# Kernel optimization log

Measured on AMD Instinct MI355X. Metric: run time of the kernel, lower is better.

The kernel has to match this reference:

```python
import jax, jax.numpy as jnp
import numpy as np

B, L, H_IN = 2, 512, 768
E = 256          # hidden_size
N = 12           # num_labels


def setup_inputs() -> dict:
    key = jax.random.key(0)
    ks = jax.random.split(key, 10)
    lim_in = 1.0 / np.sqrt(H_IN)
    lim_e = 1.0 / np.sqrt(E)
    lim_2e = 1.0 / np.sqrt(2 * E)
    return {
        "x":    jax.random.normal(ks[0], (B, L, H_IN), dtype=jnp.float32),
        "sW":   jax.random.uniform(ks[1], (E, H_IN), jnp.float32, -lim_in, lim_in),
        "sb":   jax.random.uniform(ks[2], (E,), jnp.float32, -lim_in, lim_in),
        "tW":   jax.random.uniform(ks[3], (E, H_IN), jnp.float32, -lim_in, lim_in),
        "tb":   jax.random.uniform(ks[4], (E,), jnp.float32, -lim_in, lim_in),
        "f2W":  jax.random.uniform(ks[5], (E, 2 * E), jnp.float32, -lim_2e, lim_2e),
        "f2b":  jax.random.uniform(ks[6], (E,), jnp.float32, -lim_2e, lim_2e),
        "f3W":  jax.random.normal(ks[7], (N, E), dtype=jnp.float32),  # init_weights: normal_
        "f3b":  jax.random.uniform(ks[8], (N,), jnp.float32, -lim_e, lim_e),
        "blW":  jax.random.normal(ks[9], (E * N, E), dtype=jnp.float32),  # bi_linear, no bias
    }


def reference(x, sW, sb, tW, tb, f2W, f2b, f3W, f3b, blW):
    b, l, _ = x.shape
    s = jax.nn.relu(x @ sW.T + sb)  # [B,L,E]
    t = jax.nn.relu(x @ tW.T + tb)  # [B,L,E]
    # biaffine term: key[b,s,e,n] = (s @ blW.T) reshaped, then key @ t^T
    key = (s @ blW.T).reshape(b, l, E, N)             # [B,L,E,N]
    out1 = jnp.einsum('bsen,ble->bsnl', key, t)       # [B,S,N,L]
    # pairwise concat-MLP, decomposed: cat(u,v) @ f2W.T == u@Wu.T + v@Wv.T
    Wu, Wv = f2W[:, :E], f2W[:, E:]
    su = s @ Wu.T                                     # [B,L,E]
    tv = t @ Wv.T                                     # [B,L,E]
    h = jax.nn.relu(su[:, :, None, :] + tv[:, None, :, :] + f2b)  # [B,L,L,E]
    out2 = h @ f3W.T + f3b                            # [B,L,L,N]
    out2 = jnp.transpose(out2, (0, 1, 3, 2))          # [B,L,N,L]
    return out1 + out2
```

## Files before the change

kernel.cpp:

```cpp
#include <hip/hip_runtime.h>
#include <hip/hip_bf16.h>


typedef unsigned short u16;
typedef __attribute__((ext_vector_type(8))) short    s16x8;
typedef __attribute__((ext_vector_type(8))) _Float16 f16x8;
typedef __attribute__((ext_vector_type(4))) float    f32x4;

__device__ inline u16 f2h(float f) { return __builtin_bit_cast(u16, (_Float16)f); }

__device__ inline s16x8 cvt2(float4 a, float4 b) {
    f16x8 h;
    h[0] = (_Float16)a.x; h[1] = (_Float16)a.y; h[2] = (_Float16)a.z; h[3] = (_Float16)a.w;
    h[4] = (_Float16)b.x; h[5] = (_Float16)b.y; h[6] = (_Float16)b.z; h[7] = (_Float16)b.w;
    return __builtin_bit_cast(s16x8, h);
}

__device__ inline f16x8 relu8(f16x8 v) {
#if __has_builtin(__builtin_elementwise_max)
    f16x8 z = {};
    return __builtin_elementwise_max(v, z);
#else
#pragma unroll
    for (int q = 0; q < 8; ++q) v[q] = v[q] > (_Float16)0.f ? v[q] : (_Float16)0.f;
    return v;
#endif
}

__device__ inline f32x4 mfma_f16(s16x8 a, s16x8 b, f32x4 c) {
    return __builtin_amdgcn_mfma_f32_16x16x32_f16(
        __builtin_bit_cast(f16x8, a), __builtin_bit_cast(f16x8, b), c, 0, 0, 0);
}
__device__ inline f32x4 mfma_f16v(f16x8 a, s16x8 b, f32x4 c) {
    return __builtin_amdgcn_mfma_f32_16x16x32_f16(a, __builtin_bit_cast(f16x8, b), c, 0, 0, 0);
}

__global__ __launch_bounds__(256, 3)
void prep_kernel(const float* __restrict__ x, const float* __restrict__ sW,
                 const float* __restrict__ tW, const float* __restrict__ sb,
                 const float* __restrict__ tb, const float* __restrict__ f2W,
                 const float* __restrict__ blW, const float* __restrict__ f3W,
                 u16* __restrict__ STb, u16* __restrict__ blkw, u16* __restrict__ f3wb)
{
    if (blockIdx.x >= 256) {
        int idx = (blockIdx.x - 256) * 256 + threadIdx.x;
        float4 v;
        u16* dst;
        if (idx < 229376) {
            int i4 = idx * 4;
            int r = i4 >> 8, k = i4 & 255;
            const float* src;
            if (r < 3072)      { int n = r >> 8, e = r & 255; src = &blW[(e * 12 + n) * 256 + k]; }
            else if (r < 3328) { src = &f2W[(r - 3072) * 512 + k]; }
            else               { src = &f2W[(r - 3328) * 512 + 256 + k]; }
            v = *(const float4*)src;
            dst = &blkw[i4];
        } else {
            int i4 = (idx - 229376) * 4;
            int row = i4 >> 8, e = i4 & 255;
            if (row < 12) v = *(const float4*)&f3W[row * 256 + e];
            else          v = make_float4(0.f, 0.f, 0.f, 0.f);
            dst = &f3wb[i4];
        }
        ushort4 o;
        o.x = f2h(v.x); o.y = f2h(v.y); o.z = f2h(v.z); o.w = f2h(v.w);
        *(ushort4*)dst = o;
        return;
    }
    __shared__ u16 As[64 * 72];
    __shared__ u16 Bs[32 * 72];
    const int tid = threadIdx.x;
    const int g = blockIdx.x;
    const int xcd = g & 7, slot = g >> 3;
    const int m0 = (((xcd << 1) | (slot >> 4))) * 64;
    const int n0 = (slot & 15) * 32;
    const int w = tid >> 6, l = tid & 63;
    const int wr = (w >> 1) * 32, wc = (w & 1) * 16;
    const int lr = l & 15, lg = l >> 4;
    const int srow = tid >> 2, kq = tid & 3;

    const float* ap = &x[(size_t)(m0 + srow) * 768 + kq * 16];
    const bool bstg = (tid < 128);
    const float* bp = nullptr;
    if (bstg) {
        int br = n0 + (tid >> 2);
        bp = (br < 256) ? &sW[(size_t)br * 768 + kq * 16]
                        : &tW[(size_t)(br - 256) * 768 + kq * 16];
    }
    float4 ra0 = *(const float4*)(ap + 0),  ra1 = *(const float4*)(ap + 4);
    float4 ra2 = *(const float4*)(ap + 8),  ra3 = *(const float4*)(ap + 12);
    float4 rb0, rb1, rb2, rb3;
    if (bstg) {
        rb0 = *(const float4*)(bp + 0);  rb1 = *(const float4*)(bp + 4);
        rb2 = *(const float4*)(bp + 8);  rb3 = *(const float4*)(bp + 12);
    }

    f32x4 acc[2] = {};
    for (int k0 = 0; k0 < 768; k0 += 64) {
        __syncthreads();
        *(s16x8*)&As[srow * 72 + kq * 16]     = cvt2(ra0, ra1);
        *(s16x8*)&As[srow * 72 + kq * 16 + 8] = cvt2(ra2, ra3);
        if (bstg) {
            *(s16x8*)&Bs[(tid >> 2) * 72 + kq * 16]     = cvt2(rb0, rb1);
            *(s16x8*)&Bs[(tid >> 2) * 72 + kq * 16 + 8] = cvt2(rb2, rb3);
        }
        __syncthreads();
        if (k0 + 64 < 768) {
            ra0 = *(const float4*)(ap + k0 + 64 + 0);  ra1 = *(const float4*)(ap + k0 + 64 + 4);
            ra2 = *(const float4*)(ap + k0 + 64 + 8);  ra3 = *(const float4*)(ap + k0 + 64 + 12);
            if (bstg) {
                rb0 = *(const float4*)(bp + k0 + 64 + 0);  rb1 = *(const float4*)(bp + k0 + 64 + 4);
                rb2 = *(const float4*)(bp + k0 + 64 + 8);  rb3 = *(const float4*)(bp + k0 + 64 + 12);
            }
        }
#pragma unroll
        for (int kk = 0; kk < 64; kk += 32) {
            s16x8 af[2], bf;
            af[0] = *(const s16x8*)&As[(wr      + lr) * 72 + kk + lg * 8];
            af[1] = *(const s16x8*)&As[(wr + 16 + lr) * 72 + kk + lg * 8];
            bf    = *(const s16x8*)&Bs[(wc      + lr) * 72 + kk + lg * 8];
            acc[0] = mfma_f16(af[0], bf, acc[0]);
            acc[1] = mfma_f16(af[1], bf, acc[1]);
        }
    }
#pragma unroll
    for (int fi = 0; fi < 2; ++fi) {
#pragma unroll
        for (int r = 0; r < 4; ++r) {
            int grow = m0 + wr + fi * 16 + lg * 4 + r;
            int gcol = n0 + wc + lr;
            float bias = (gcol < 256) ? sb[gcol] : tb[gcol - 256];
            float v = fmaxf(acc[fi][r] + bias, 0.f);
            STb[(size_t)grow * 512 + gcol] = f2h(v);
        }
    }
}

__global__ __launch_bounds__(256, 6)
void gemm_kst(const u16* __restrict__ STb, const u16* __restrict__ BLKW,
              const float* __restrict__ f2b,
              u16* __restrict__ KEYF, u16* __restrict__ SUp, u16* __restrict__ TVp)
{
    __shared__ u16 As[64 * 72];
    __shared__ u16 Bs[64 * 72];
    const int tid = threadIdx.x;
    const int lin = blockIdx.x + blockIdx.y * 56;
    const int xcd = lin & 7, slot = lin >> 3;
    const int n0 = (xcd * 7 + (slot >> 4)) * 64;
    const int m0 = (slot & 15) * 64;
    const int w = tid >> 6, l = tid & 63;
    const int wr = (w >> 1) * 32, wc = (w & 1) * 32;
    const int lr = l & 15, lg = l >> 4;
    const int srow = tid >> 2, kq = tid & 3;

    const u16* A = STb + (n0 >= 3328 ? 256 : 0);
    const u16* ap = &A[(size_t)(m0 + srow) * 512];
    const u16* bp = &BLKW[(size_t)(n0 + srow) * 256];
    s16x8 ra0 = *(const s16x8*)&ap[kq * 8];
    s16x8 ra1 = *(const s16x8*)&ap[(kq + 4) * 8];
    s16x8 rb0 = *(const s16x8*)&bp[kq * 8];
    s16x8 rb1 = *(const s16x8*)&bp[(kq + 4) * 8];

    f32x4 acc[2][2] = {};
    for (int k0 = 0; k0 < 256; k0 += 64) {
        __syncthreads();
        *(s16x8*)&As[srow * 72 + kq * 8]       = ra0;
        *(s16x8*)&As[srow * 72 + (kq + 4) * 8] = ra1;
        *(s16x8*)&Bs[srow * 72 + kq * 8]       = rb0;
        *(s16x8*)&Bs[srow * 72 + (kq + 4) * 8] = rb1;
        __syncthreads();
        if (k0 + 64 < 256) {
            ra0 = *(const s16x8*)&ap[k0 + 64 + kq * 8];
            ra1 = *(const s16x8*)&ap[k0 + 64 + (kq + 4) * 8];
            rb0 = *(const s16x8*)&bp[k0 + 64 + kq * 8];
            rb1 = *(const s16x8*)&bp[k0 + 64 + (kq + 4) * 8];
        }
#pragma unroll
        for (int kk = 0; kk < 64; kk += 32) {
            s16x8 af[2], bf[2];
            af[0] = *(const s16x8*)&As[(wr      + lr) * 72 + kk + lg * 8];
            af[1] = *(const s16x8*)&As[(wr + 16 + lr) * 72 + kk + lg * 8];
            bf[0] = *(const s16x8*)&Bs[(wc      + lr) * 72 + kk + lg * 8];
            bf[1] = *(const s16x8*)&Bs[(wc + 16 + lr) * 72 + kk + lg * 8];
#pragma unroll
            for (int fi = 0; fi < 2; ++fi)
#pragma unroll
                for (int fj = 0; fj < 2; ++fj)
                    acc[fi][fj] = mfma_f16(af[fi], bf[fj], acc[fi][fj]);
        }
    }
#pragma unroll
    for (int fi = 0; fi < 2; ++fi) {
#pragma unroll
        for (int fj = 0; fj < 2; ++fj) {
#pragma unroll
            for (int r = 0; r < 4; ++r) {
                int grow = m0 + wr + fi * 16 + lg * 4 + r;
                int gcol = n0 + wc + fj * 16 + lr;
                float v = acc[fi][fj][r];
                if (gcol < 3072) {
                    int n = gcol >> 8, e = gcol & 255;
                    int g = grow >> 4, li = grow & 15;
                    int it = e >> 5, sub = (e >> 3) & 3, eo = e & 7;
                    KEYF[((((size_t)n * 64 + g) * 8 + it) * 64 + sub * 16 + li) * 8 + eo] = f2h(v);
                } else if (gcol < 3328) {
                    SUp[(size_t)grow * 256 + (gcol - 3072)] = f2h(v);
                } else {
                    TVp[(size_t)grow * 256 + (gcol - 3328)] = f2h(v + f2b[gcol - 3328]);
                }
            }
        }
    }
}

__global__ __launch_bounds__(256, 4)
void fused_out(const u16* __restrict__ KEYF, const u16* __restrict__ STb,
               const u16* __restrict__ SUp, const u16* __restrict__ TVp,
               const u16* __restrict__ F3WH, const float* __restrict__ f3b,
               float* __restrict__ out)
{
    __shared__ __align__(16) char smem[27904];
    u16* lds = (u16*)smem;
    const int TC0 = 0, SUC0 = 2560, TVC0 = 3840, F3C = 6400;

    const int tid = threadIdx.x;
    const int w = tid >> 6, l = tid & 63;

    const int lin  = blockIdx.x + (blockIdx.y << 4) + (blockIdx.z << 9);
    const int orig = (lin & 7) * 128 + (lin >> 3);
    const int j0 = (orig & 15) * 32;
    const int i0 = ((orig >> 4) & 31) * 16;
    const int b  = orig >> 9;

    const int lr = l & 15, lg = l >> 4;

    const u16* src1; int d1;
    if (tid < 128) {
        int jj = tid >> 2, qq = tid & 3;
        src1 = STb + (size_t)(b * 512 + j0 + jj) * 512 + 256 + qq * 8;
        d1 = TC0 + jj * 40 + qq * 8;
    } else {
        int q = tid - 128, jj = q >> 2, qq = q & 3;
        src1 = TVp + (size_t)(b * 512 + j0 + jj) * 256 + qq * 8;
        d1 = TVC0 + jj * 40 + qq * 8;
    }
    const u16* src2 = nullptr; int d2 = 0;
    const bool has2 = (tid < 64);
    if (has2) {
        int ii = tid >> 2, qq = tid & 3;
        src2 = SUp + (size_t)(b * 512 + i0 + ii) * 256 + qq * 8;
        d2 = SUC0 + ii * 40 + qq * 8;
    }

#pragma unroll
    for (int rr = 0; rr < 2; ++rr) {
        int g = tid + 256 * rr;
        int row = g >> 5, qq = g & 31;
        *(s16x8*)&lds[F3C + row * 264 + qq * 8] = *(const s16x8*)&F3WH[row * 256 + qq * 8];
    }

    const int gblk = b * 32 + (i0 >> 4);
    const u16* kfb0 = KEYF + ((size_t)((3 * w + 0) * 64 + gblk) * 8) * 512 + l * 8;
    const u16* kfb1 = KEYF + ((size_t)((3 * w + 1) * 64 + gblk) * 8) * 512 + l * 8;
    const u16* kfb2 = KEYF + ((size_t)((3 * w + 2) * 64 + gblk) * 8) * 512 + l * 8;

    s16x8 r1 = *(const s16x8*)src1;
    s16x8 r2 = {};
    if (has2) r2 = *(const s16x8*)src2;
    *(s16x8*)&lds[d1] = r1;
    if (has2) *(s16x8*)&lds[d2] = r2;
    s16x8 kf0 = *(const s16x8*)kfb0;
    s16x8 kf1 = *(const s16x8*)kfb1;
    s16x8 kf2 = *(const s16x8*)kfb2;
    r1 = *(const s16x8*)(src1 + 32);
    if (has2) r2 = *(const s16x8*)(src2 + 32);
    __syncthreads();

    f32x4 acc1[3][2] = {};
    f32x4 acc2[8]    = {};

#pragma unroll
    for (int it = 0; it < 8; ++it) {
        const int cur = it & 1, nxt = cur ^ 1;
        if (it < 7) {
            *(s16x8*)&lds[d1 + nxt * 1280] = r1;
            if (has2) *(s16x8*)&lds[d2 + nxt * 640] = r2;
        }
        s16x8 tf0 = *(const s16x8*)&lds[TC0 + cur * 1280 + lr * 40 + lg * 8];
        s16x8 tf1 = *(const s16x8*)&lds[TC0 + cur * 1280 + (16 + lr) * 40 + lg * 8];
        acc1[0][0] = mfma_f16(kf0, tf0, acc1[0][0]);
        acc1[0][1] = mfma_f16(kf0, tf1, acc1[0][1]);
        acc1[1][0] = mfma_f16(kf1, tf0, acc1[1][0]);
        acc1[1][1] = mfma_f16(kf1, tf1, acc1[1][1]);
        acc1[2][0] = mfma_f16(kf2, tf0, acc1[2][0]);
        acc1[2][1] = mfma_f16(kf2, tf1, acc1[2][1]);
        s16x8 nk0, nk1, nk2;
        if (it < 7) {
            nk0 = *(const s16x8*)(kfb0 + (it + 1) * 512);
            nk1 = *(const s16x8*)(kfb1 + (it + 1) * 512);
            nk2 = *(const s16x8*)(kfb2 + (it + 1) * 512);
        }
        f16x8 sv = __builtin_bit_cast(f16x8,
            *(const s16x8*)&lds[SUC0 + cur * 640 + lr * 40 + lg * 8]);
        s16x8 f3fr = *(const s16x8*)&lds[F3C + lr * 264 + it * 32 + lg * 8];
#pragma unroll
        for (int jj = 0; jj < 8; ++jj) {
            int j = w * 8 + jj;
            f16x8 tv8 = __builtin_bit_cast(f16x8,
                *(const s16x8*)&lds[TVC0 + cur * 1280 + j * 40 + lg * 8]);
            f16x8 hv = relu8(sv + tv8);
            acc2[jj] = mfma_f16v(hv, f3fr, acc2[jj]);
        }
        if (it < 6) {
            r1 = *(const s16x8*)(src1 + (it + 2) * 32);
            if (has2) r2 = *(const s16x8*)(src2 + (it + 2) * 32);
        }
        if (it < 7) { kf0 = nk0; kf1 = nk1; kf2 = nk2; }
        __syncthreads();
    }

    float* mg = (float*)smem;
    if (lr < 12) {
#pragma unroll
        for (int r = 0; r < 4; ++r) {
            int i = lg * 4 + r;
            f32x4 v0, v1;
            v0[0] = acc2[0][r]; v0[1] = acc2[1][r]; v0[2] = acc2[2][r]; v0[3] = acc2[3][r];
            v1[0] = acc2[4][r]; v1[1] = acc2[5][r]; v1[2] = acc2[6][r]; v1[3] = acc2[7][r];
            *(f32x4*)&mg[lr * 580 + i * 36 + w * 8]     = v0;
            *(f32x4*)&mg[lr * 580 + i * 36 + w * 8 + 4] = v1;
        }
    }
    __syncthreads();
#pragma unroll
    for (int a = 0; a < 3; ++a) {
        int n = 3 * w + a;
        float fb = f3b[n];
#pragma unroll
        for (int fj = 0; fj < 2; ++fj) {
            int j = fj * 16 + lr;
#pragma unroll
            for (int r = 0; r < 4; ++r) {
                int i = lg * 4 + r;
                float vv = acc1[a][fj][r] + mg[n * 580 + i * 36 + j] + fb;
                out[(((size_t)(b * 512 + i0 + i)) * 12 + n) * 512 + j0 + j] = vv;
            }
        }
    }
}

extern "C" void kernel_launch(void* const* d_in, const int* in_sizes, int n_in,
                              void* d_out, int out_size, void* d_ws, size_t ws_size,
                              hipStream_t stream)
{
    const float* x   = (const float*)d_in[0];
    const float* sW  = (const float*)d_in[1];
    const float* sb  = (const float*)d_in[2];
    const float* tW  = (const float*)d_in[3];
    const float* tb  = (const float*)d_in[4];
    const float* f2W = (const float*)d_in[5];
    const float* f2b = (const float*)d_in[6];
    const float* f3W = (const float*)d_in[7];
    const float* f3b = (const float*)d_in[8];
    const float* blW = (const float*)d_in[9];
    float* out = (float*)d_out;

    char* p = (char*)d_ws;
    u16* STb   = (u16*)p; p += 1048576;
    u16* blkw  = (u16*)p; p += 1835008;
    u16* KEYF  = (u16*)p; p += 6291456;
    u16* SUp   = (u16*)p; p += 524288;
    u16* TVp   = (u16*)p; p += 524288;
    u16* f3wbg = (u16*)p; p += 8192;

    prep_kernel<<<1156, 256, 0, stream>>>(x, sW, tW, sb, tb, f2W, blW, f3W,
                                          STb, blkw, f3wbg);
    gemm_kst<<<dim3(56, 16), 256, 0, stream>>>(STb, blkw, f2b, KEYF, SUp, TVp);
    fused_out<<<dim3(16, 32, 2), 256, 0, stream>>>(KEYF, STb, SUp, TVp, f3wbg, f3b, out);
}
```

Baseline: 42.71 us.

## Widen fused_out tile to 64 columns with 512-thread blocks

The fused output kernel now uses 512 threads per block and covers 64 j-columns instead of 32. The eight waves split into two j-halves that share the same KEYF fragments, which halves the number of blocks and the redundant loads of KEYF, SUp and F3W. The merge through LDS is done in two passes of 6 labels each so it fits in the enlarged shared buffer. The cost is more LDS per block, extra barriers in the epilogue, and possibly lower occupancy under the 512x4 launch bound.

```diff
diff --git a/kernel.cpp b/kernel.cpp
--- a/kernel.cpp
+++ b/kernel.cpp
@@ -200,9 +200,9 @@
                 float v = acc[fi][fj][r];
                 if (gcol < 3072) {
                     int n = gcol >> 8, e = gcol & 255;
-                    int g = grow >> 4, li = grow & 15;
+                    int g2 = grow >> 4, li = grow & 15;
                     int it = e >> 5, sub = (e >> 3) & 3, eo = e & 7;
-                    KEYF[((((size_t)n * 64 + g) * 8 + it) * 64 + sub * 16 + li) * 8 + eo] = f2h(v);
+                    KEYF[((((size_t)n * 64 + g2) * 8 + it) * 64 + sub * 16 + li) * 8 + eo] = f2h(v);
                 } else if (gcol < 3328) {
                     SUp[(size_t)grow * 256 + (gcol - 3072)] = f2h(v);
                 } else {
@@ -213,56 +213,55 @@
     }
 }
 
-__global__ __launch_bounds__(256, 4)
+__global__ __launch_bounds__(512, 4)
 void fused_out(const u16* __restrict__ KEYF, const u16* __restrict__ STb,
                const u16* __restrict__ SUp, const u16* __restrict__ TVp,
                const u16* __restrict__ F3WH, const float* __restrict__ f3b,
                float* __restrict__ out)
 {
-    __shared__ __align__(16) char smem[27904];
+    __shared__ __align__(16) char smem[31488];
     u16* lds = (u16*)smem;
-    const int TC0 = 0, SUC0 = 2560, TVC0 = 3840, F3C = 6400;
+    const int TC0 = 0, SUC0 = 5120, TVC0 = 6400, F3C = 11520;
 
     const int tid = threadIdx.x;
     const int w = tid >> 6, l = tid & 63;
 
-    const int lin  = blockIdx.x + (blockIdx.y << 4) + (blockIdx.z << 9);
-    const int orig = (lin & 7) * 128 + (lin >> 3);
-    const int j0 = (orig & 15) * 32;
-    const int i0 = ((orig >> 4) & 31) * 16;
-    const int b  = orig >> 9;
+    const int lin  = blockIdx.x + (blockIdx.y << 3) + (blockIdx.z << 8);
+    const int orig = (lin & 7) * 64 + (lin >> 3);
+    const int j0 = (orig & 7) * 64;
+    const int i0 = ((orig >> 3) & 31) * 16;
+    const int b  = orig >> 8;
 
     const int lr = l & 15, lg = l >> 4;
+    const int wn = w & 3, jh = w >> 2;
 
     const u16* src1; int d1;
-    if (tid < 128) {
+    if (tid < 256) {
         int jj = tid >> 2, qq = tid & 3;
         src1 = STb + (size_t)(b * 512 + j0 + jj) * 512 + 256 + qq * 8;
         d1 = TC0 + jj * 40 + qq * 8;
     } else {
-        int q = tid - 128, jj = q >> 2, qq = q & 3;
+        int q = tid - 256, jj = q >> 2, qq = q & 3;
         src1 = TVp + (size_t)(b * 512 + j0 + jj) * 256 + qq * 8;
         d1 = TVC0 + jj * 40 + qq * 8;
     }
+    const bool has2 = (tid < 64);
     const u16* src2 = nullptr; int d2 = 0;
-    const bool has2 = (tid < 64);
     if (has2) {
         int ii = tid >> 2, qq = tid & 3;
         src2 = SUp + (size_t)(b * 512 + i0 + ii) * 256 + qq * 8;
         d2 = SUC0 + ii * 40 + qq * 8;
     }
 
-#pragma unroll
-    for (int rr = 0; rr < 2; ++rr) {
-        int g = tid + 256 * rr;
-        int row = g >> 5, qq = g & 31;
+    {
+        int row = tid >> 5, qq = tid & 31;
         *(s16x8*)&lds[F3C + row * 264 + qq * 8] = *(const s16x8*)&F3WH[row * 256 + qq * 8];
     }
 
     const int gblk = b * 32 + (i0 >> 4);
-    const u16* kfb0 = KEYF + ((size_t)((3 * w + 0) * 64 + gblk) * 8) * 512 + l * 8;
-    const u16* kfb1 = KEYF + ((size_t)((3 * w + 1) * 64 + gblk) * 8) * 512 + l * 8;
-    const u16* kfb2 = KEYF + ((size_t)((3 * w + 2) * 64 + gblk) * 8) * 512 + l * 8;
+    const u16* kfb0 = KEYF + ((size_t)((3 * wn + 0) * 64 + gblk) * 8) * 512 + l * 8;
+    const u16* kfb1 = KEYF + ((size_t)((3 * wn + 1) * 64 + gblk) * 8) * 512 + l * 8;
+    const u16* kfb2 = KEYF + ((size_t)((3 * wn + 2) * 64 + gblk) * 8) * 512 + l * 8;
 
     s16x8 r1 = *(const s16x8*)src1;
     s16x8 r2 = {};
@@ -283,22 +282,21 @@
     for (int it = 0; it < 8; ++it) {
         const int cur = it & 1, nxt = cur ^ 1;
         if (it < 7) {
-            *(s16x8*)&lds[d1 + nxt * 1280] = r1;
+            *(s16x8*)&lds[d1 + nxt * 2560] = r1;
             if (has2) *(s16x8*)&lds[d2 + nxt * 640] = r2;
         }
-        s16x8 tf0 = *(const s16x8*)&lds[TC0 + cur * 1280 + lr * 40 + lg * 8];
-        s16x8 tf1 = *(const s16x8*)&lds[TC0 + cur * 1280 + (16 + lr) * 40 + lg * 8];
+        s16x8 tf0 = *(const s16x8*)&lds[TC0 + cur * 2560 + (jh * 32      + lr) * 40 + lg * 8];
+        s16x8 tf1 = *(const s16x8*)&lds[TC0 + cur * 2560 + (jh * 32 + 16 + lr) * 40 + lg * 8];
         acc1[0][0] = mfma_f16(kf0, tf0, acc1[0][0]);
         acc1[0][1] = mfma_f16(kf0, tf1, acc1[0][1]);
         acc1[1][0] = mfma_f16(kf1, tf0, acc1[1][0]);
         acc1[1][1] = mfma_f16(kf1, tf1, acc1[1][1]);
         acc1[2][0] = mfma_f16(kf2, tf0, acc1[2][0]);
         acc1[2][1] = mfma_f16(kf2, tf1, acc1[2][1]);
-        s16x8 nk0, nk1, nk2;
         if (it < 7) {
-            nk0 = *(const s16x8*)(kfb0 + (it + 1) * 512);
-            nk1 = *(const s16x8*)(kfb1 + (it + 1) * 512);
-            nk2 = *(const s16x8*)(kfb2 + (it + 1) * 512);
+            kf0 = *(const s16x8*)(kfb0 + (it + 1) * 512);
+            kf1 = *(const s16x8*)(kfb1 + (it + 1) * 512);
+            kf2 = *(const s16x8*)(kfb2 + (it + 1) * 512);
         }
         f16x8 sv = __builtin_bit_cast(f16x8,
             *(const s16x8*)&lds[SUC0 + cur * 640 + lr * 40 + lg * 8]);
@@ -307,7 +305,7 @@
         for (int jj = 0; jj < 8; ++jj) {
             int j = w * 8 + jj;
             f16x8 tv8 = __builtin_bit_cast(f16x8,
-                *(const s16x8*)&lds[TVC0 + cur * 1280 + j * 40 + lg * 8]);
+                *(const s16x8*)&lds[TVC0 + cur * 2560 + j * 40 + lg * 8]);
             f16x8 hv = relu8(sv + tv8);
             acc2[jj] = mfma_f16v(hv, f3fr, acc2[jj]);
         }
@@ -315,35 +313,42 @@
             r1 = *(const s16x8*)(src1 + (it + 2) * 32);
             if (has2) r2 = *(const s16x8*)(src2 + (it + 2) * 32);
         }
-        if (it < 7) { kf0 = nk0; kf1 = nk1; kf2 = nk2; }
         __syncthreads();
     }
 
     float* mg = (float*)smem;
-    if (lr < 12) {
-#pragma unroll
-        for (int r = 0; r < 4; ++r) {
-            int i = lg * 4 + r;
-            f32x4 v0, v1;
-            v0[0] = acc2[0][r]; v0[1] = acc2[1][r]; v0[2] = acc2[2][r]; v0[3] = acc2[3][r];
-            v1[0] = acc2[4][r]; v1[1] = acc2[5][r]; v1[2] = acc2[6][r]; v1[3] = acc2[7][r];
-            *(f32x4*)&mg[lr * 580 + i * 36 + w * 8]     = v0;
-            *(f32x4*)&mg[lr * 580 + i * 36 + w * 8 + 4] = v1;
-        }
-    }
-    __syncthreads();
-#pragma unroll
-    for (int a = 0; a < 3; ++a) {
-        int n = 3 * w + a;
-        float fb = f3b[n];
-#pragma unroll
-        for (int fj = 0; fj < 2; ++fj) {
-            int j = fj * 16 + lr;
+#pragma unroll
+    for (int nc = 0; nc < 2; ++nc) {
+        __syncthreads();
+        const int nb = nc * 6;
+        const int lrp = lr - nb;
+        if (lrp >= 0 && lrp < 6) {
 #pragma unroll
             for (int r = 0; r < 4; ++r) {
                 int i = lg * 4 + r;
-                float vv = acc1[a][fj][r] + mg[n * 580 + i * 36 + j] + fb;
-                out[(((size_t)(b * 512 + i0 + i)) * 12 + n) * 512 + j0 + j] = vv;
+                f32x4 v0, v1;
+                v0[0] = acc2[0][r]; v0[1] = acc2[1][r]; v0[2] = acc2[2][r]; v0[3] = acc2[3][r];
+                v1[0] = acc2[4][r]; v1[1] = acc2[5][r]; v1[2] = acc2[6][r]; v1[3] = acc2[7][r];
+                *(f32x4*)&mg[lrp * 1092 + i * 68 + w * 8]     = v0;
+                *(f32x4*)&mg[lrp * 1092 + i * 68 + w * 8 + 4] = v1;
+            }
+        }
+        __syncthreads();
+        if ((wn >> 1) == nc) {
+#pragma unroll
+            for (int a = 0; a < 3; ++a) {
+                int n = 3 * wn + a;
+                float fb = f3b[n];
+#pragma unroll
+                for (int fj = 0; fj < 2; ++fj) {
+                    int j = jh * 32 + fj * 16 + lr;
+#pragma unroll
+                    for (int r = 0; r < 4; ++r) {
+                        int i = lg * 4 + r;
+                        float vv = acc1[a][fj][r] + mg[(n - nb) * 1092 + i * 68 + j] + fb;
+                        out[(((size_t)(b * 512 + i0 + i)) * 12 + n) * 512 + j0 + j] = vv;
+                    }
+                }
             }
         }
     }
@@ -376,5 +381,5 @@
     prep_kernel<<<1156, 256, 0, stream>>>(x, sW, tW, sb, tb, f2W, blW, f3W,
                                           STb, blkw, f3wbg);
     gemm_kst<<<dim3(56, 16), 256, 0, stream>>>(STb, blkw, f2b, KEYF, SUp, TVp);
-    fused_out<<<dim3(16, 32, 2), 256, 0, stream>>>(KEYF, STb, SUp, TVp, f3wbg, f3b, out);
-}
+    fused_out<<<dim3(8, 32, 2), 512, 0, stream>>>(KEYF, STb, SUp, TVp, f3wbg, f3b, out);
+}
```

Result: no change. 42.74 us, median of 3 (+0.1%).
